# Performance work log

Measured on AMD Instinct MI355X. Metric: run time of the kernel, lower is better.

Reference implementation:

```python
import itertools
import jax, jax.numpy as jnp
import numpy as np

VOLSHAPE = (160, 192, 160)  # D, H, W (SynthSeg-style 3D crop)
NDIMS = 3
BATCH = 4
CHANNELS = 1


def setup_inputs() -> dict:
    key = jax.random.key(0)
    k1, k2 = jax.random.split(key)
    vol = jax.random.normal(k1, (BATCH, *VOLSHAPE, CHANNELS), dtype=jnp.float32)
    # affine near identity: layer treats trf as (roughly) the full 4x4 matrix applied
    # to centered coordinates; affine_to_shift subtracts the centered mesh.
    trf = jnp.eye(NDIMS + 1, dtype=jnp.float32)[None] \
        + 0.05 * jax.random.normal(k2, (BATCH, NDIMS + 1, NDIMS + 1), dtype=jnp.float32)
    return {"vol": vol, "trf": trf}


def _meshgrid(volshape):
    ranges = [jnp.arange(s, dtype=jnp.float32) for s in volshape]
    return jnp.stack(jnp.meshgrid(*ranges, indexing='ij'), axis=-1)  # [D,H,W,3]


def _affine_to_shift(A, volshape):
    # A: [4,4]; faithful to neuron.utils.affine_to_shift with shift_center=True
    mesh = _meshgrid(volshape)                                        # [D,H,W,3]
    center = jnp.array([(s - 1) / 2.0 for s in volshape], dtype=jnp.float32)
    mesh_c = mesh - center                                            # centered mesh
    flat = mesh_c.reshape(-1, NDIMS)                                  # [V,3]
    flat1 = jnp.concatenate([flat, jnp.ones((flat.shape[0], 1), flat.dtype)], axis=1)  # [V,4]
    loc = flat1 @ A[:NDIMS].T                                         # [V,3] = (A[:3] @ mesh^T)^T
    return loc.reshape(*volshape, NDIMS) - mesh_c                     # shift field


def _interpn_linear(vol, loc):
    # vol: [D,H,W,C]; loc: [D,H,W,3] absolute sample locations
    volshape = vol.shape[:-1]
    C = vol.shape[-1]
    max_loc = jnp.array([d - 1 for d in volshape], dtype=jnp.float32)
    loc0 = jnp.floor(loc)
    clipped = jnp.clip(loc, 0.0, max_loc)
    loc0c = jnp.clip(loc0, 0.0, max_loc)
    loc1c = jnp.clip(loc0c + 1.0, 0.0, max_loc)
    d1 = loc1c - clipped           # weight for corner bit 0 (neuron's reversed ordering)
    d0 = 1.0 - d1                  # weight for corner bit 1
    i0 = loc0c.astype(jnp.int32)
    i1 = loc1c.astype(jnp.int32)
    strides = np.array([volshape[1] * volshape[2], volshape[2], 1], dtype=np.int32)
    vol_flat = vol.reshape(-1, C)
    out = jnp.zeros((*volshape, C), dtype=vol.dtype)
    for corner in itertools.product((0, 1), repeat=NDIMS):
        idx = jnp.zeros(volshape, dtype=jnp.int32)
        wt = jnp.ones(volshape, dtype=vol.dtype)
        for d in range(NDIMS):
            ii = (i0 if corner[d] == 0 else i1)[..., d]
            idx = idx + ii * int(strides[d])
            wt = wt * (d1 if corner[d] == 0 else d0)[..., d]
        gathered = vol_flat[idx.reshape(-1)].reshape(*volshape, C)
        out = out + wt[..., None] * gathered
    return out


def reference(vol, trf):
    volshape = vol.shape[1:-1]

    def single(v, A):
        shift = _affine_to_shift(A, volshape)          # affine -> dense shift field
        loc = _meshgrid(volshape) + shift              # transform(): mesh + shift
        return _interpn_linear(v, loc)

    return jax.vmap(single)(vol, trf)
```

## Files before the change

kernel.cpp:

```cpp
#include <hip/hip_runtime.h>

constexpr int D = 160, H = 192, W = 160, B = 4;
constexpr int V  = D * H * W;
constexpr int HW = H * W;
constexpr int VPT = 4;
constexpr int TW  = 32, TH = 8;
constexpr int GXW = W / TW;
constexpr int GXH = H / TH;
constexpr int SD_CAP = 10, SH_CAP = 12, SW_CAP = 40;
constexpr int PLANE = SH_CAP * SW_CAP;
constexpr int LDS_FLOATS = SD_CAP * PLANE;

struct DimS { int i0; float w0; };

__device__ __forceinline__ DimS prep(float loc, float maxv, int maxi) {
    float c  = __builtin_amdgcn_fmed3f(loc, 0.0f, maxv);
    int  i0  = min((int)c, maxi - 1);
    DimS s;
    s.i0 = i0;
    s.w0 = (float)(i0 + 1) - c;
    return s;
}

__device__ __forceinline__ float lerp3(DimS sd, DimS sh, DimS sw,
                                       float2 v00, float2 v01,
                                       float2 v10, float2 v11) {
    const float pd00 = fmaf(sw.w0, v00.x - v00.y, v00.y);
    const float pd01 = fmaf(sw.w0, v01.x - v01.y, v01.y);
    const float pd10 = fmaf(sw.w0, v10.x - v10.y, v10.y);
    const float pd11 = fmaf(sw.w0, v11.x - v11.y, v11.y);
    const float q0 = fmaf(sh.w0, pd00 - pd01, pd01);
    const float q1 = fmaf(sh.w0, pd10 - pd11, pd11);
    return fmaf(sd.w0, q0 - q1, q1);
}

__device__ __forceinline__ float trilerp_g(const float* __restrict__ vb,
                                           DimS sd, DimS sh, DimS sw) {
    const float* p0 = vb + ((sd.i0 * H + sh.i0) * W + sw.i0);
    float2 v00, v01, v10, v11;
    __builtin_memcpy(&v00, p0,          8);
    __builtin_memcpy(&v01, p0 + W,      8);
    __builtin_memcpy(&v10, p0 + HW,     8);
    __builtin_memcpy(&v11, p0 + HW + W, 8);
    return lerp3(sd, sh, sw, v00, v01, v10, v11);
}

__device__ __forceinline__ void gload_lds_row(const float* g, float* l) {
    __builtin_amdgcn_global_load_lds(
        (const __attribute__((address_space(1))) void*)g,
        (__attribute__((address_space(3))) void*)l,
        4, 0, 0);
}

__global__ __launch_bounds__(256) void st_affine_kernel(
        const float* __restrict__ vol, const float* __restrict__ trf,
        float* __restrict__ out) {
    __shared__ float sm[LDS_FLOATS];

    const int b  = blockIdx.z;
    const int d0 = blockIdx.y * VPT;
    const int hblk = blockIdx.x / GXW;
    const int wblk = blockIdx.x - hblk * GXW;
    const int w0 = wblk * TW, h0 = hblk * TH;

    const float* __restrict__ A = trf + b * 16;
    const float a00 = A[0], a01 = A[1], a02 = A[2],  a03 = A[3];
    const float a10 = A[4], a11 = A[5], a12 = A[6],  a13 = A[7];
    const float a20 = A[8], a21 = A[9], a22 = A[10], a23 = A[11];

    constexpr float cd = (D - 1) * 0.5f;
    constexpr float ch = (H - 1) * 0.5f;
    constexpr float cw = (W - 1) * 0.5f;

    const float md0 = (float)d0 - cd, mh0 = (float)h0 - ch, mw0 = (float)w0 - cw;
    const float od = cd + fmaf(a00, md0, fmaf(a01, mh0, fmaf(a02, mw0, a03)));
    const float oh = ch + fmaf(a10, md0, fmaf(a11, mh0, fmaf(a12, mw0, a13)));
    const float ow = cw + fmaf(a20, md0, fmaf(a21, mh0, fmaf(a22, mw0, a23)));

    const float Ed = (float)(VPT - 1), Eh = (float)(TH - 1), Ew = (float)(TW - 1);
    const float dn = od + fminf(a00*Ed,0.f) + fminf(a01*Eh,0.f) + fminf(a02*Ew,0.f);
    const float dx = od + fmaxf(a00*Ed,0.f) + fmaxf(a01*Eh,0.f) + fmaxf(a02*Ew,0.f);
    const float hn = oh + fminf(a10*Ed,0.f) + fminf(a11*Eh,0.f) + fminf(a12*Ew,0.f);
    const float hx = oh + fmaxf(a10*Ed,0.f) + fmaxf(a11*Eh,0.f) + fmaxf(a12*Ew,0.f);
    const float wn = ow + fminf(a20*Ed,0.f) + fminf(a21*Eh,0.f) + fminf(a22*Ew,0.f);
    const float wx = ow + fmaxf(a20*Ed,0.f) + fmaxf(a21*Eh,0.f) + fmaxf(a22*Ew,0.f);

    const int lo_d = min((int)__builtin_amdgcn_fmed3f(dn, 0.f, (float)(D-1)), D - 2);
    const int hi_d = min((int)__builtin_amdgcn_fmed3f(dx, 0.f, (float)(D-1)), D - 2) + 1;
    const int lo_h = min((int)__builtin_amdgcn_fmed3f(hn, 0.f, (float)(H-1)), H - 2);
    const int hi_h = min((int)__builtin_amdgcn_fmed3f(hx, 0.f, (float)(H-1)), H - 2) + 1;
    const int lo_w = min((int)__builtin_amdgcn_fmed3f(wn, 0.f, (float)(W-1)), W - 2);
    const int hi_w = min((int)__builtin_amdgcn_fmed3f(wx, 0.f, (float)(W-1)), W - 2) + 1;
    const int SDn = hi_d - lo_d + 1;
    const int SHn = hi_h - lo_h + 1;
    const int SWn = hi_w - lo_w + 1;

    const float fy = (float)threadIdx.y, fx = (float)threadIdx.x;
    float ld = fmaf(a01, fy, fmaf(a02, fx, od));
    float lh = fmaf(a11, fy, fmaf(a12, fx, oh));
    float lw = fmaf(a21, fy, fmaf(a22, fx, ow));

    const float* __restrict__ vb = vol + (size_t)b * V;
    float* __restrict__ ob = out + (size_t)b * V + (size_t)d0 * HW;
    const int oofs = (h0 + threadIdx.y) * W + w0 + threadIdx.x;

    if (SDn <= SD_CAP && SHn <= SH_CAP && SWn <= SW_CAP) {
        const int tid  = threadIdx.y * TW + threadIdx.x;
        const int wv   = tid >> 6;
        const int lane = tid & 63;
        const bool act = lane < SWn;
        const float* gz = vb + (size_t)lo_d * HW + (size_t)lo_h * W + lo_w;
        float* lz = sm;
        for (int z = 0; z < SDn; ++z) {
            for (int y = wv; y < SHn; y += 4) {
                if (act)
                    gload_lds_row(gz + (size_t)y * W + lane, lz + y * SW_CAP);
            }
            gz += HW;
            lz += PLANE;
        }
        __syncthreads();

        const int offL = (lo_d * SH_CAP + lo_h) * SW_CAP + lo_w;
#pragma unroll
        for (int k = 0; k < VPT; ++k) {
            const DimS sd = prep(ld, (float)(D - 1), D - 1);
            const DimS sh = prep(lh, (float)(H - 1), H - 1);
            const DimS sw = prep(lw, (float)(W - 1), W - 1);
            const int idx = (sd.i0 * SH_CAP + sh.i0) * SW_CAP + sw.i0 - offL;
            const float2 v00 = make_float2(sm[idx],                  sm[idx + 1]);
            const float2 v01 = make_float2(sm[idx + SW_CAP],         sm[idx + SW_CAP + 1]);
            const float2 v10 = make_float2(sm[idx + PLANE],          sm[idx + PLANE + 1]);
            const float2 v11 = make_float2(sm[idx + PLANE + SW_CAP], sm[idx + PLANE + SW_CAP + 1]);
            const float r = lerp3(sd, sh, sw, v00, v01, v10, v11);
            __builtin_nontemporal_store(r, ob + oofs + k * HW);
            ld += a00; lh += a10; lw += a20;
        }
    } else {
#pragma unroll
        for (int k = 0; k < VPT; ++k) {
            const DimS sd = prep(ld, (float)(D - 1), D - 1);
            const DimS sh = prep(lh, (float)(H - 1), H - 1);
            const DimS sw = prep(lw, (float)(W - 1), W - 1);
            const float r = trilerp_g(vb, sd, sh, sw);
            __builtin_nontemporal_store(r, ob + oofs + k * HW);
            ld += a00; lh += a10; lw += a20;
        }
    }
}

extern "C" void kernel_launch(void* const* d_in, const int* in_sizes, int n_in,
                              void* d_out, int out_size, void* d_ws, size_t ws_size,
                              hipStream_t stream) {
    const float* vol = (const float*)d_in[0];
    const float* trf = (const float*)d_in[1];
    float* out = (float*)d_out;

    dim3 grid(GXH * GXW, D / VPT, B);
    dim3 block(TW, TH, 1);
    st_affine_kernel<<<grid, block, 0, stream>>>(vol, trf, out);
}
```

Before: 151.1 us.

## Double-buffer LDS staging across four depth chunks per block

Each block now handles four consecutive depth chunks and double-buffers the LDS source tile. The global-to-LDS load for chunk c+1 is issued before chunk c is interpolated, using explicit vmcnt waits and barriers, so load latency overlaps with compute. Staging is unrolled to a fixed size with clamped indices, so it always issues the full row count, and the grid shrinks by four. This adds LDS use (two buffers) and redundant loads, and the hand-counted vmcnt values are fragile if the fallback path or the compiler's memory ops change the count.

```diff
diff --git a/kernel.cpp b/kernel.cpp
--- a/kernel.cpp
+++ b/kernel.cpp
@@ -4,12 +4,15 @@
 constexpr int V  = D * H * W;
 constexpr int HW = H * W;
 constexpr int VPT = 4;
+constexpr int NC  = 4;
 constexpr int TW  = 32, TH = 8;
 constexpr int GXW = W / TW;
 constexpr int GXH = H / TH;
 constexpr int SD_CAP = 10, SH_CAP = 12, SW_CAP = 40;
 constexpr int PLANE = SH_CAP * SW_CAP;
-constexpr int LDS_FLOATS = SD_CAP * PLANE;
+constexpr int CHUNK_FLOATS = SD_CAP * PLANE;
+constexpr int STAGE_LOADS = SD_CAP * 3;
+constexpr int STORES_PER_CHUNK = VPT;
 
 struct DimS { int i0; float w0; };
 
@@ -52,13 +55,13 @@
         4, 0, 0);
 }
 
-__global__ __launch_bounds__(256) void st_affine_kernel(
+__global__ __launch_bounds__(256, 4) void st_affine_kernel(
         const float* __restrict__ vol, const float* __restrict__ trf,
         float* __restrict__ out) {
-    __shared__ float sm[LDS_FLOATS];
+    __shared__ float sm[2][CHUNK_FLOATS];
 
     const int b  = blockIdx.z;
-    const int d0 = blockIdx.y * VPT;
+    const int dbase = blockIdx.y * (VPT * NC);
     const int hblk = blockIdx.x / GXW;
     const int wblk = blockIdx.x - hblk * GXW;
     const int w0 = wblk * TW, h0 = hblk * TH;
@@ -72,80 +75,127 @@
     constexpr float ch = (H - 1) * 0.5f;
     constexpr float cw = (W - 1) * 0.5f;
 
-    const float md0 = (float)d0 - cd, mh0 = (float)h0 - ch, mw0 = (float)w0 - cw;
+    const float md0 = (float)dbase - cd, mh0 = (float)h0 - ch, mw0 = (float)w0 - cw;
     const float od = cd + fmaf(a00, md0, fmaf(a01, mh0, fmaf(a02, mw0, a03)));
     const float oh = ch + fmaf(a10, md0, fmaf(a11, mh0, fmaf(a12, mw0, a13)));
     const float ow = cw + fmaf(a20, md0, fmaf(a21, mh0, fmaf(a22, mw0, a23)));
 
     const float Ed = (float)(VPT - 1), Eh = (float)(TH - 1), Ew = (float)(TW - 1);
-    const float dn = od + fminf(a00*Ed,0.f) + fminf(a01*Eh,0.f) + fminf(a02*Ew,0.f);
-    const float dx = od + fmaxf(a00*Ed,0.f) + fmaxf(a01*Eh,0.f) + fmaxf(a02*Ew,0.f);
-    const float hn = oh + fminf(a10*Ed,0.f) + fminf(a11*Eh,0.f) + fminf(a12*Ew,0.f);
-    const float hx = oh + fmaxf(a10*Ed,0.f) + fmaxf(a11*Eh,0.f) + fmaxf(a12*Ew,0.f);
-    const float wn = ow + fminf(a20*Ed,0.f) + fminf(a21*Eh,0.f) + fminf(a22*Ew,0.f);
-    const float wx = ow + fmaxf(a20*Ed,0.f) + fmaxf(a21*Eh,0.f) + fmaxf(a22*Ew,0.f);
-
-    const int lo_d = min((int)__builtin_amdgcn_fmed3f(dn, 0.f, (float)(D-1)), D - 2);
-    const int hi_d = min((int)__builtin_amdgcn_fmed3f(dx, 0.f, (float)(D-1)), D - 2) + 1;
-    const int lo_h = min((int)__builtin_amdgcn_fmed3f(hn, 0.f, (float)(H-1)), H - 2);
-    const int hi_h = min((int)__builtin_amdgcn_fmed3f(hx, 0.f, (float)(H-1)), H - 2) + 1;
-    const int lo_w = min((int)__builtin_amdgcn_fmed3f(wn, 0.f, (float)(W-1)), W - 2);
-    const int hi_w = min((int)__builtin_amdgcn_fmed3f(wx, 0.f, (float)(W-1)), W - 2) + 1;
-    const int SDn = hi_d - lo_d + 1;
-    const int SHn = hi_h - lo_h + 1;
-    const int SWn = hi_w - lo_w + 1;
+    const float dn_off = fminf(a00*Ed,0.f) + fminf(a01*Eh,0.f) + fminf(a02*Ew,0.f);
+    const float dx_off = fmaxf(a00*Ed,0.f) + fmaxf(a01*Eh,0.f) + fmaxf(a02*Ew,0.f);
+    const float hn_off = fminf(a10*Ed,0.f) + fminf(a11*Eh,0.f) + fminf(a12*Ew,0.f);
+    const float hx_off = fmaxf(a10*Ed,0.f) + fmaxf(a11*Eh,0.f) + fmaxf(a12*Ew,0.f);
+    const float wn_off = fminf(a20*Ed,0.f) + fminf(a21*Eh,0.f) + fminf(a22*Ew,0.f);
+    const float wx_off = fmaxf(a20*Ed,0.f) + fmaxf(a21*Eh,0.f) + fmaxf(a22*Ew,0.f);
+
+    const int tid  = threadIdx.y * TW + threadIdx.x;
+    const int wv   = tid >> 6;
+    const int lane = tid & 63;
+    const float* __restrict__ vb = vol + (size_t)b * V;
+
+    auto mkinfo = [&](float odc, float ohc, float owc,
+                      int& lod, int& loh, int& low, bool& fit,
+                      int& SDc, int& SHc, int& SWc) {
+        const int ld_ = min((int)__builtin_amdgcn_fmed3f(odc + dn_off, 0.f, (float)(D-1)), D-2);
+        const int hd_ = min((int)__builtin_amdgcn_fmed3f(odc + dx_off, 0.f, (float)(D-1)), D-2) + 1;
+        const int lh_ = min((int)__builtin_amdgcn_fmed3f(ohc + hn_off, 0.f, (float)(H-1)), H-2);
+        const int hh_ = min((int)__builtin_amdgcn_fmed3f(ohc + hx_off, 0.f, (float)(H-1)), H-2) + 1;
+        const int lw_ = min((int)__builtin_amdgcn_fmed3f(owc + wn_off, 0.f, (float)(W-1)), W-2);
+        const int hw_ = min((int)__builtin_amdgcn_fmed3f(owc + wx_off, 0.f, (float)(W-1)), W-2) + 1;
+        const int SDn = hd_ - ld_ + 1, SHn = hh_ - lh_ + 1, SWn = hw_ - lw_ + 1;
+        fit = (SDn <= SD_CAP) && (SHn <= SH_CAP) && (SWn <= SW_CAP);
+        SDc = min(SDn, SD_CAP); SHc = min(SHn, SH_CAP); SWc = min(SWn, SW_CAP);
+        lod = ld_; loh = lh_; low = lw_;
+    };
+
+    auto stage = [&](float* lbuf, int lod, int loh, int low,
+                     int SDc, int SHc, int SWc) {
+        const bool act = lane < SWc;
+        const float* gz = vb + (size_t)lod * HW + (size_t)loh * W + low;
+#pragma unroll
+        for (int z = 0; z < SD_CAP; ++z) {
+            const float* gp = gz + (size_t)min(z, SDc - 1) * HW;
+            float* lp = lbuf + z * PLANE;
+#pragma unroll
+            for (int t = 0; t < 3; ++t) {
+                const int y  = wv + t * 4;
+                const int ys = min(y, SHc - 1);
+                if (act) gload_lds_row(gp + (size_t)ys * W + lane, lp + y * SW_CAP);
+            }
+        }
+    };
+
+    int lo_d[2], lo_h[2], lo_w[2];
+    bool fits[2];
+    float odc = od, ohc = oh, owc = ow;
+    const float st_d = VPT * a00, st_h = VPT * a10, st_w = VPT * a20;
+    {
+        int SDc, SHc, SWc;
+        mkinfo(odc, ohc, owc, lo_d[0], lo_h[0], lo_w[0], fits[0], SDc, SHc, SWc);
+        stage(sm[0], lo_d[0], lo_h[0], lo_w[0], SDc, SHc, SWc);
+    }
+    __builtin_amdgcn_sched_barrier(0);
+    asm volatile("s_waitcnt vmcnt(0)" ::: "memory");
+    __builtin_amdgcn_s_barrier();
+    __builtin_amdgcn_sched_barrier(0);
 
     const float fy = (float)threadIdx.y, fx = (float)threadIdx.x;
     float ld = fmaf(a01, fy, fmaf(a02, fx, od));
     float lh = fmaf(a11, fy, fmaf(a12, fx, oh));
     float lw = fmaf(a21, fy, fmaf(a22, fx, ow));
 
-    const float* __restrict__ vb = vol + (size_t)b * V;
-    float* __restrict__ ob = out + (size_t)b * V + (size_t)d0 * HW;
-    const int oofs = (h0 + threadIdx.y) * W + w0 + threadIdx.x;
-
-    if (SDn <= SD_CAP && SHn <= SH_CAP && SWn <= SW_CAP) {
-        const int tid  = threadIdx.y * TW + threadIdx.x;
-        const int wv   = tid >> 6;
-        const int lane = tid & 63;
-        const bool act = lane < SWn;
-        const float* gz = vb + (size_t)lo_d * HW + (size_t)lo_h * W + lo_w;
-        float* lz = sm;
-        for (int z = 0; z < SDn; ++z) {
-            for (int y = wv; y < SHn; y += 4) {
-                if (act)
-                    gload_lds_row(gz + (size_t)y * W + lane, lz + y * SW_CAP);
+    float* obk = out + (size_t)b * V + (size_t)dbase * HW
+               + (size_t)(h0 + threadIdx.y) * W + (w0 + threadIdx.x);
+
+#pragma unroll
+    for (int c = 0; c < NC; ++c) {
+        if (c + 1 < NC) {
+            odc += st_d; ohc += st_h; owc += st_w;
+            int SDc, SHc, SWc;
+            const int p = (c + 1) & 1;
+            mkinfo(odc, ohc, owc, lo_d[p], lo_h[p], lo_w[p], fits[p], SDc, SHc, SWc);
+            stage(sm[p], lo_d[p], lo_h[p], lo_w[p], SDc, SHc, SWc);
+            __builtin_amdgcn_sched_barrier(0);
+            asm volatile("s_waitcnt vmcnt(34)" ::: "memory");
+        } else {
+            __builtin_amdgcn_sched_barrier(0);
+            asm volatile("s_waitcnt vmcnt(4)" ::: "memory");
+        }
+        __builtin_amdgcn_s_barrier();
+        __builtin_amdgcn_sched_barrier(0);
+
+        const float* lb = sm[c & 1];
+        if (fits[c & 1]) {
+            const int offL = (lo_d[c & 1] * SH_CAP + lo_h[c & 1]) * SW_CAP + lo_w[c & 1];
+#pragma unroll
+            for (int k = 0; k < VPT; ++k) {
+                const DimS sd = prep(ld, (float)(D - 1), D - 1);
+                const DimS sh = prep(lh, (float)(H - 1), H - 1);
+                const DimS sw = prep(lw, (float)(W - 1), W - 1);
+                const int idx = (sd.i0 * SH_CAP + sh.i0) * SW_CAP + sw.i0 - offL;
+                const float2 v00 = make_float2(lb[idx],                  lb[idx + 1]);
+                const float2 v01 = make_float2(lb[idx + SW_CAP],         lb[idx + SW_CAP + 1]);
+                const float2 v10 = make_float2(lb[idx + PLANE],          lb[idx + PLANE + 1]);
+                const float2 v11 = make_float2(lb[idx + PLANE + SW_CAP], lb[idx + PLANE + SW_CAP + 1]);
+                const float r = lerp3(sd, sh, sw, v00, v01, v10, v11);
+                __builtin_nontemporal_store(r, obk);
+                obk += HW;
+                ld += a00; lh += a10; lw += a20;
             }
-            gz += HW;
-            lz += PLANE;
+        } else {
+#pragma unroll
+            for (int k = 0; k < VPT; ++k) {
+                const DimS sd = prep(ld, (float)(D - 1), D - 1);
+                const DimS sh = prep(lh, (float)(H - 1), H - 1);
+                const DimS sw = prep(lw, (float)(W - 1), W - 1);
+                const float r = trilerp_g(vb, sd, sh, sw);
+                __builtin_nontemporal_store(r, obk);
+                obk += HW;
+                ld += a00; lh += a10; lw += a20;
+            }
         }
-        __syncthreads();
-
-        const int offL = (lo_d * SH_CAP + lo_h) * SW_CAP + lo_w;
-#pragma unroll
-        for (int k = 0; k < VPT; ++k) {
-            const DimS sd = prep(ld, (float)(D - 1), D - 1);
-            const DimS sh = prep(lh, (float)(H - 1), H - 1);
-            const DimS sw = prep(lw, (float)(W - 1), W - 1);
-            const int idx = (sd.i0 * SH_CAP + sh.i0) * SW_CAP + sw.i0 - offL;
-            const float2 v00 = make_float2(sm[idx],                  sm[idx + 1]);
-            const float2 v01 = make_float2(sm[idx + SW_CAP],         sm[idx + SW_CAP + 1]);
-            const float2 v10 = make_float2(sm[idx + PLANE],          sm[idx + PLANE + 1]);
-            const float2 v11 = make_float2(sm[idx + PLANE + SW_CAP], sm[idx + PLANE + SW_CAP + 1]);
-            const float r = lerp3(sd, sh, sw, v00, v01, v10, v11);
-            __builtin_nontemporal_store(r, ob + oofs + k * HW);
-            ld += a00; lh += a10; lw += a20;
-        }
-    } else {
-#pragma unroll
-        for (int k = 0; k < VPT; ++k) {
-            const DimS sd = prep(ld, (float)(D - 1), D - 1);
-            const DimS sh = prep(lh, (float)(H - 1), H - 1);
-            const DimS sw = prep(lw, (float)(W - 1), W - 1);
-            const float r = trilerp_g(vb, sd, sh, sw);
-            __builtin_nontemporal_store(r, ob + oofs + k * HW);
-            ld += a00; lh += a10; lw += a20;
-        }
+        __builtin_amdgcn_s_barrier();
+        __builtin_amdgcn_sched_barrier(0);
     }
 }
 
@@ -156,7 +206,7 @@
     const float* trf = (const float*)d_in[1];
     float* out = (float*)d_out;
 
-    dim3 grid(GXH * GXW, D / VPT, B);
+    dim3 grid(GXH * GXW, D / (VPT * NC), B);
     dim3 block(TW, TH, 1);
     st_affine_kernel<<<grid, block, 0, stream>>>(vol, trf, out);
 }
```

Result: slower. 159.9 us (+5.8%).
